# Kernel tuning notes

Measured on AMD Instinct MI355X. Metric: run time of the kernel, lower is better.

## Reference

```python
import jax, jax.numpy as jnp
import numpy as np

DIM = 180
HEADS = 6
WIN = 12
NGS = 2304          # num_gs_seed -> gs len
SQ = 48             # sqrt(num_gs_seed)
B = 64              # window-batch
TABLE = (2 * max(SQ, WIN) - 1) ** 2  # 9025 rows in bias table


def _rel_pos_index():
    # Mirrors the torch __init__ buffer construction (np.unique gives the
    # deterministic sorted-unique indexing the original intends).
    cs = (np.indices((SQ, SQ)) + 0.5) * WIN          # [2, SQ, SQ]
    ct = (np.indices((WIN, WIN)) + 0.5) * SQ
    d = cs.reshape(2, -1)[:, :, None] - ct.reshape(2, -1)[:, None, :]
    _, inv = np.unique(d.flatten(), return_inverse=True)
    idx = inv.reshape(d.shape).astype(np.int64)
    idx[0] *= idx.max()
    return jnp.asarray(idx.sum(0), dtype=jnp.int32)


def setup_inputs() -> dict:
    key = jax.random.key(0)
    ks = jax.random.split(key, 12)
    std = 0.02
    d = DIM
    inp = {
        "gs": jax.random.normal(ks[0], (B, NGS, d), dtype=jnp.float32),
        "feat": jax.random.normal(ks[1], (B, WIN * WIN, d), dtype=jnp.float32),
        "Wq": jax.random.normal(ks[2], (d, d), dtype=jnp.float32) * std,
        "bq": jnp.zeros((d,), dtype=jnp.float32),
        "Wk": jax.random.normal(ks[3], (d, d), dtype=jnp.float32) * std,
        "bk": jnp.zeros((d,), dtype=jnp.float32),
        "Wv": jax.random.normal(ks[4], (d, d), dtype=jnp.float32) * std,
        "bv": jnp.zeros((d,), dtype=jnp.float32),
        "Wp": jax.random.normal(ks[5], (d, d), dtype=jnp.float32) * std,
        "bp": jnp.zeros((d,), dtype=jnp.float32),
        "bias_table": jax.random.normal(ks[6], (TABLE, HEADS), dtype=jnp.float32) * std,
        "rel_pos_index": _rel_pos_index(),
    }
    return inp


def reference(gs, feat, Wq, bq, Wk, bk, Wv, bv, Wp, bp, bias_table, rel_pos_index):
    b, ng, c = gs.shape
    n = feat.shape[1]
    hd = c // HEADS
    scale = hd ** (-0.5)

    q = (gs @ Wq + bq).reshape(b, ng, HEADS, hd).transpose(0, 2, 1, 3) * scale  # [b,H,ng,hd]
    k = (feat @ Wk + bk).reshape(b, n, HEADS, hd).transpose(0, 2, 1, 3)          # [b,H,n,hd]
    v = (feat @ Wv + bv).reshape(b, n, HEADS, hd).transpose(0, 2, 1, 3)

    attn = jnp.einsum('bhqd,bhkd->bhqk', q, k)                                    # [b,H,ng,n]
    bias = bias_table[rel_pos_index]                                              # [ng,n,H]
    attn = attn + jnp.transpose(bias, (2, 0, 1))[None]                            # broadcast over b
    attn = jax.nn.softmax(attn, axis=-1)

    x = jnp.einsum('bhqk,bhkd->bhqd', attn, v)                                    # [b,H,ng,hd]
    x = x.transpose(0, 2, 1, 3).reshape(b, ng, c)
    return x @ Wp + bp
```

## Files before the change

kernel.cpp:

```cpp
#include <hip/hip_runtime.h>

#define DIM   180
#define HEADS 6
#define HD    30
#define NKEY  144
#define NGS   2304
#define BATCH 64
#define TQ    64
#define QT    (NGS / TQ)
#define WPAD  192
#define SXS   200
#define SQS   200
#define SPS   152
#define SVS   152
#define SKS   40
#define KB_STRIDE (NKEY * SKS)
#define VB_STRIDE (32 * SVS)

typedef unsigned short u16;
typedef short v8s __attribute__((ext_vector_type(8)));
typedef float v4f __attribute__((ext_vector_type(4)));

__device__ __forceinline__ float bf2f(u16 u) {
    union { unsigned int i; float f; } w; w.i = ((unsigned int)u) << 16; return w.f;
}
__device__ __forceinline__ u16 f2bf(float f) {
    union { float f; unsigned int i; } w; w.f = f;
    unsigned int r = w.i + 0x7fffu + ((w.i >> 16) & 1u);
    return (u16)(r >> 16);
}

__global__ __launch_bounds__(256) void wt_prep_kernel(
    const float* __restrict__ Wq, const float* __restrict__ Wp,
    u16* __restrict__ WqT, u16* __restrict__ WpT) {
    int idx = blockIdx.x * 256 + threadIdx.x;
    int sel = idx >= WPAD * WPAD;
    int rr  = sel ? idx - WPAD * WPAD : idx;
    int j = rr / WPAD, k = rr - j * WPAD;
    const float* W = sel ? Wp : Wq;
    u16* T = sel ? WpT : WqT;
    float v = (j < DIM && k < DIM) ? W[k * DIM + j] : 0.f;
    T[j * WPAD + k] = f2bf(v);
}

__global__ __launch_bounds__(256) void gather_bias_kernel(
    const float* __restrict__ table, const int* __restrict__ rpi,
    u16* __restrict__ biasg) {
    int idx = blockIdx.x * 256 + threadIdx.x;
    int r = rpi[idx];
    int q = idx / NKEY, n = idx - q * NKEY;
#pragma unroll
    for (int h = 0; h < HEADS; ++h)
        biasg[((size_t)h * NGS + q) * NKEY + n] = f2bf(table[r * HEADS + h]);
}

__global__ __launch_bounds__(256) void kv_proj_kernel(
    const float* __restrict__ feat,
    const float* __restrict__ Wk, const float* __restrict__ bk,
    const float* __restrict__ Wv, const float* __restrict__ bv,
    u16* __restrict__ Kb, u16* __restrict__ VbT) {
    __shared__ float sF[16 * DIM];
    int b  = blockIdx.x / 9;
    int n0 = (blockIdx.x % 9) * 16;
    int tid = threadIdx.x;
    {
        const float4* src = (const float4*)(feat + (size_t)(b * NKEY + n0) * DIM);
        float4* dst = (float4*)sF;
        for (int i = tid; i < 16 * 45; i += 256) dst[i] = src[i];
    }
    __syncthreads();
    int j = tid;
    if (j < DIM) {
        float ak[16], av[16];
#pragma unroll
        for (int r = 0; r < 16; ++r) { ak[r] = 0.f; av[r] = 0.f; }
        const float4* sF4 = (const float4*)sF;
        for (int kc = 0; kc < 45; ++kc) {
            int kk = kc * 4;
            float wk0 = Wk[(kk + 0) * DIM + j], wk1 = Wk[(kk + 1) * DIM + j];
            float wk2 = Wk[(kk + 2) * DIM + j], wk3 = Wk[(kk + 3) * DIM + j];
            float wv0 = Wv[(kk + 0) * DIM + j], wv1 = Wv[(kk + 1) * DIM + j];
            float wv2 = Wv[(kk + 2) * DIM + j], wv3 = Wv[(kk + 3) * DIM + j];
#pragma unroll
            for (int r = 0; r < 16; ++r) {
                float4 g = sF4[r * 45 + kc];
                ak[r] = fmaf(g.x, wk0, ak[r]); ak[r] = fmaf(g.y, wk1, ak[r]);
                ak[r] = fmaf(g.z, wk2, ak[r]); ak[r] = fmaf(g.w, wk3, ak[r]);
                av[r] = fmaf(g.x, wv0, av[r]); av[r] = fmaf(g.y, wv1, av[r]);
                av[r] = fmaf(g.z, wv2, av[r]); av[r] = fmaf(g.w, wv3, av[r]);
            }
        }
        int h = j / 30, d = j - 30 * h;
        u16* kp = Kb  + (size_t)(b * HEADS + h) * KB_STRIDE;
        u16* vp = VbT + (size_t)(b * HEADS + h) * VB_STRIDE;
        float bkj = bk[j], bvj = bv[j];
#pragma unroll
        for (int r = 0; r < 16; ++r) {
            kp[(n0 + r) * SKS + d] = f2bf(ak[r] + bkj);
            vp[d * SVS + n0 + r]   = f2bf(av[r] + bvj);
        }
    }
}

__global__ __launch_bounds__(256, 2) void attn_kernel(
    const float* __restrict__ gs,
    const u16* __restrict__ WqT, const float* __restrict__ bq,
    const u16* __restrict__ WpT, const float* __restrict__ bp,
    const u16* __restrict__ Kb, const u16* __restrict__ VbT,
    const u16* __restrict__ biasg, float* __restrict__ out) {

    __shared__ u16 sX[TQ * SXS];
    __shared__ u16 sQ[TQ * SQS];
    __shared__ u16 sP[TQ * SPS];
    __shared__ u16 sV[32 * SVS];

    const int tid  = threadIdx.x;
    const int w    = tid >> 6;
    const int l15  = tid & 15;
    const int quad = (tid >> 4) & 3;
    const int b    = blockIdx.x / QT;
    const int q0   = (blockIdx.x % QT) * TQ;
    const float SCALE = 0.18257418583505536f;

    {
        const float4* src = (const float4*)(gs + (size_t)(b * NGS + q0) * DIM);
        for (int i = tid; i < TQ * 45; i += 256) {
            int row = i / 45, c = i - row * 45;
            float4 g = src[row * 45 + c];
            unsigned lo = (unsigned)f2bf(g.x) | ((unsigned)f2bf(g.y) << 16);
            unsigned hi = (unsigned)f2bf(g.z) | ((unsigned)f2bf(g.w) << 16);
            *(uint2*)&sX[row * SXS + c * 4] = make_uint2(lo, hi);
        }
        for (int i = tid; i < TQ * 16; i += 256)
            sX[(i >> 4) * SXS + 180 + (i & 15)] = 0;
    }
    __syncthreads();

    {
        v4f acc[12];
#pragma unroll
        for (int i = 0; i < 12; ++i) acc[i] = (v4f){0.f, 0.f, 0.f, 0.f};
        for (int kt = 0; kt < 6; ++kt) {
            v8s A[4];
#pragma unroll
            for (int m = 0; m < 4; ++m)
                A[m] = *(const v8s*)&sX[(16 * m + l15) * SXS + kt * 32 + quad * 8];
#pragma unroll
            for (int jj = 0; jj < 3; ++jj) {
                int j0 = (3 * w + jj) * 16;
                v8s B = *(const v8s*)&WqT[(size_t)(j0 + l15) * WPAD + kt * 32 + quad * 8];
#pragma unroll
                for (int m = 0; m < 4; ++m)
                    acc[jj * 4 + m] = __builtin_amdgcn_mfma_f32_16x16x32_bf16(
                        A[m], B, acc[jj * 4 + m], 0, 0, 0);
            }
        }
#pragma unroll
        for (int jj = 0; jj < 3; ++jj) {
            int j = (3 * w + jj) * 16 + l15;
            if (j < DIM) {
                int h = j / 30;
                int pos = j + 2 * h;
                float bqj = bq[j];
#pragma unroll
                for (int m = 0; m < 4; ++m)
#pragma unroll
                    for (int r = 0; r < 4; ++r)
                        sQ[(16 * m + quad * 4 + r) * SQS + pos] =
                            f2bf((acc[jj * 4 + m][r] + bqj) * SCALE);
            }
        }
    }
    for (int i = tid; i < TQ * HEADS * 2; i += 256) {
        int row = i / 12, c = i - row * 12;
        sQ[row * SQS + (c >> 1) * 32 + 30 + (c & 1)] = 0;
    }
    __syncthreads();

    for (int h = 0; h < HEADS; ++h) {
        {
            const uint4* ks = (const uint4*)(Kb + (size_t)(b * HEADS + h) * KB_STRIDE);
            uint4* kd = (uint4*)sP;
            for (int i = tid; i < (KB_STRIDE * 2 / 16); i += 256) kd[i] = ks[i];
            const uint4* vs = (const uint4*)(VbT + (size_t)(b * HEADS + h) * VB_STRIDE);
            uint4* vd = (uint4*)sV;
            for (int i = tid; i < (VB_STRIDE * 2 / 16); i += 256) vd[i] = vs[i];
        }
        __syncthreads();

        v8s qa = *(const v8s*)&sQ[(16 * w + l15) * SQS + h * 32 + quad * 8];
        v4f la[9];
        const u16* bg = biasg + ((size_t)h * NGS + q0 + 16 * w + quad * 4) * NKEY + l15;
#pragma unroll
        for (int t = 0; t < 9; ++t) {
            v4f c;
#pragma unroll
            for (int r = 0; r < 4; ++r) c[r] = bf2f(bg[r * NKEY + t * 16]);
            v8s kb = *(const v8s*)&sP[(16 * t + l15) * SKS + quad * 8];
            la[t] = __builtin_amdgcn_mfma_f32_16x16x32_bf16(qa, kb, c, 0, 0, 0);
        }

        float mx[4], sm[4];
#pragma unroll
        for (int r = 0; r < 4; ++r) {
            float m = la[0][r];
#pragma unroll
            for (int t = 1; t < 9; ++t) m = fmaxf(m, la[t][r]);
            m = fmaxf(m, __shfl_xor(m, 1));
            m = fmaxf(m, __shfl_xor(m, 2));
            m = fmaxf(m, __shfl_xor(m, 4));
            m = fmaxf(m, __shfl_xor(m, 8));
            mx[r] = m; sm[r] = 0.f;
        }
#pragma unroll
        for (int t = 0; t < 9; ++t)
#pragma unroll
            for (int r = 0; r < 4; ++r) {
                la[t][r] = __expf(la[t][r] - mx[r]);
                sm[r] += la[t][r];
            }
#pragma unroll
        for (int r = 0; r < 4; ++r) {
            sm[r] += __shfl_xor(sm[r], 1);
            sm[r] += __shfl_xor(sm[r], 2);
            sm[r] += __shfl_xor(sm[r], 4);
            sm[r] += __shfl_xor(sm[r], 8);
            sm[r] = 1.f / sm[r];
        }
        __syncthreads();

#pragma unroll
        for (int t = 0; t < 9; ++t)
#pragma unroll
            for (int r = 0; r < 4; ++r)
                sP[(16 * w + quad * 4 + r) * SPS + 16 * t + l15] = f2bf(la[t][r] * sm[r]);
        __syncthreads();

        v4f x0 = (v4f){0.f, 0.f, 0.f, 0.f}, x1 = x0;
        for (int kt = 0; kt < 5; ++kt) {
            v8s pa, vb0, vb1;
            if (kt == 4 && quad >= 2) {
                pa = (v8s){0,0,0,0,0,0,0,0}; vb0 = pa; vb1 = pa;
            } else {
                pa  = *(const v8s*)&sP[(16 * w + l15) * SPS + kt * 32 + quad * 8];
                vb0 = *(const v8s*)&sV[l15 * SVS + kt * 32 + quad * 8];
                vb1 = *(const v8s*)&sV[(16 + l15) * SVS + kt * 32 + quad * 8];
            }
            x0 = __builtin_amdgcn_mfma_f32_16x16x32_bf16(pa, vb0, x0, 0, 0, 0);
            x1 = __builtin_amdgcn_mfma_f32_16x16x32_bf16(pa, vb1, x1, 0, 0, 0);
        }
#pragma unroll
        for (int r = 0; r < 4; ++r) {
            int qrow = (16 * w + quad * 4 + r) * SXS + h * 30;
            sX[qrow + l15] = f2bf(x0[r]);
            if (l15 < 14) sX[qrow + 16 + l15] = f2bf(x1[r]);
        }
        __syncthreads();
    }

    {
        v4f acc[12];
#pragma unroll
        for (int i = 0; i < 12; ++i) acc[i] = (v4f){0.f, 0.f, 0.f, 0.f};
        for (int kt = 0; kt < 6; ++kt) {
            v8s A[4];
#pragma unroll
            for (int m = 0; m < 4; ++m)
                A[m] = *(const v8s*)&sX[(16 * m + l15) * SXS + kt * 32 + quad * 8];
#pragma unroll
            for (int jj = 0; jj < 3; ++jj) {
                int j0 = (3 * w + jj) * 16;
                v8s B = *(const v8s*)&WpT[(size_t)(j0 + l15) * WPAD + kt * 32 + quad * 8];
#pragma unroll
                for (int m = 0; m < 4; ++m)
                    acc[jj * 4 + m] = __builtin_amdgcn_mfma_f32_16x16x32_bf16(
                        A[m], B, acc[jj * 4 + m], 0, 0, 0);
            }
        }
#pragma unroll
        for (int jj = 0; jj < 3; ++jj) {
            int j = (3 * w + jj) * 16 + l15;
            if (j < DIM) {
                float bpj = bp[j];
#pragma unroll
                for (int m = 0; m < 4; ++m)
#pragma unroll
                    for (int r = 0; r < 4; ++r)
                        out[(size_t)(b * NGS + q0 + 16 * m + quad * 4 + r) * DIM + j] =
                            acc[jj * 4 + m][r] + bpj;
            }
        }
    }
}

extern "C" void kernel_launch(void* const* d_in, const int* in_sizes, int n_in,
                              void* d_out, int out_size, void* d_ws, size_t ws_size,
                              hipStream_t stream) {
    const float* gs    = (const float*)d_in[0];
    const float* feat  = (const float*)d_in[1];
    const float* Wq    = (const float*)d_in[2];
    const float* bq    = (const float*)d_in[3];
    const float* Wk    = (const float*)d_in[4];
    const float* bk    = (const float*)d_in[5];
    const float* Wv    = (const float*)d_in[6];
    const float* bv    = (const float*)d_in[7];
    const float* Wp    = (const float*)d_in[8];
    const float* bp    = (const float*)d_in[9];
    const float* table = (const float*)d_in[10];
    const int*   rpi   = (const int*)d_in[11];
    float* out = (float*)d_out;

    u16* WqT   = (u16*)d_ws;
    u16* WpT   = WqT + WPAD * WPAD;
    u16* Kb    = WpT + WPAD * WPAD;
    u16* VbT   = Kb  + (size_t)BATCH * HEADS * KB_STRIDE;
    u16* biasg = VbT + (size_t)BATCH * HEADS * VB_STRIDE;

    size_t zero_bytes = (size_t)BATCH * HEADS * (KB_STRIDE + VB_STRIDE) * sizeof(u16);
    hipMemsetAsync(Kb, 0, zero_bytes, stream);

    wt_prep_kernel<<<dim3(2 * WPAD * WPAD / 256), dim3(256), 0, stream>>>(Wq, Wp, WqT, WpT);
    gather_bias_kernel<<<dim3(NGS * NKEY / 256), dim3(256), 0, stream>>>(table, rpi, biasg);
    kv_proj_kernel<<<dim3(BATCH * 9), dim3(256), 0, stream>>>(feat, Wk, bk, Wv, bv, Kb, VbT);
    attn_kernel<<<dim3(BATCH * QT), dim3(256), 0, stream>>>(
        gs, WqT, bq, WpT, bp, Kb, VbT, biasg, out);
}
```

Before: 447.1 us.

## Read K/V from global directly, transpose attention MFMA, pre-tile bias in fragment order

```diff
diff --git a/kernel.cpp b/kernel.cpp
--- a/kernel.cpp
+++ b/kernel.cpp
@@ -7,15 +7,14 @@
 #define NGS   2304
 #define BATCH 64
 #define TQ    64
-#define QT    (NGS / TQ)
+#define QT    36
 #define WPAD  192
 #define SXS   200
-#define SQS   200
 #define SPS   152
-#define SVS   152
-#define SKS   40
-#define KB_STRIDE (NKEY * SKS)
-#define VB_STRIDE (32 * SVS)
+#define KROW  40
+#define VROW  144
+#define KB_STRIDE (NKEY * KROW)
+#define VB_STRIDE (32 * VROW)
 
 typedef unsigned short u16;
 typedef short v8s __attribute__((ext_vector_type(8)));
@@ -28,6 +27,12 @@
     union { float f; unsigned int i; } w; w.f = f;
     unsigned int r = w.i + 0x7fffu + ((w.i >> 16) & 1u);
     return (u16)(r >> 16);
+}
+__device__ __forceinline__ uint2 pack4(const v4f& x) {
+    uint2 r;
+    r.x = (unsigned)f2bf(x[0]) | ((unsigned)f2bf(x[1]) << 16);
+    r.y = (unsigned)f2bf(x[2]) | ((unsigned)f2bf(x[3]) << 16);
+    return r;
 }
 
 __global__ __launch_bounds__(256) void wt_prep_kernel(
@@ -37,21 +42,35 @@
     int sel = idx >= WPAD * WPAD;
     int rr  = sel ? idx - WPAD * WPAD : idx;
     int j = rr / WPAD, k = rr - j * WPAD;
-    const float* W = sel ? Wp : Wq;
-    u16* T = sel ? WpT : WqT;
-    float v = (j < DIM && k < DIM) ? W[k * DIM + j] : 0.f;
-    T[j * WPAD + k] = f2bf(v);
+    float v;
+    if (!sel) {
+        v = (j < DIM && k < DIM) ? Wq[k * DIM + j] : 0.f;
+        WqT[j * WPAD + k] = f2bf(v);
+    } else {
+        int h = k >> 5, dd = k & 31;
+        v = (j < DIM && dd < HD) ? Wp[(h * HD + dd) * DIM + j] : 0.f;
+        WpT[j * WPAD + k] = f2bf(v);
+    }
 }
 
 __global__ __launch_bounds__(256) void gather_bias_kernel(
     const float* __restrict__ table, const int* __restrict__ rpi,
-    u16* __restrict__ biasg) {
-    int idx = blockIdx.x * 256 + threadIdx.x;
-    int r = rpi[idx];
-    int q = idx / NKEY, n = idx - q * NKEY;
-#pragma unroll
-    for (int h = 0; h < HEADS; ++h)
-        biasg[((size_t)h * NGS + q) * NKEY + n] = f2bf(table[r * HEADS + h]);
+    u16* __restrict__ biasCT) {
+    int i = blockIdx.x * 256 + threadIdx.x;
+    int lane = i & 63;
+    int tile = i >> 6;
+    int t = tile % 9;
+    int rem = tile / 9;
+    int g = rem % 144;
+    int h = rem / 144;
+    int q  = 16 * g + (lane & 15);
+    int n0 = 16 * t + (lane >> 4) * 4;
+    const int4 rr = *(const int4*)&rpi[q * NKEY + n0];
+    unsigned lo = (unsigned)f2bf(table[rr.x * HEADS + h]) |
+                  ((unsigned)f2bf(table[rr.y * HEADS + h]) << 16);
+    unsigned hi = (unsigned)f2bf(table[rr.z * HEADS + h]) |
+                  ((unsigned)f2bf(table[rr.w * HEADS + h]) << 16);
+    ((uint2*)biasCT)[i] = make_uint2(lo, hi);
 }
 
 __global__ __launch_bounds__(256) void kv_proj_kernel(
@@ -90,36 +109,36 @@
                 av[r] = fmaf(g.z, wv2, av[r]); av[r] = fmaf(g.w, wv3, av[r]);
             }
         }
-        int h = j / 30, d = j - 30 * h;
+        int h = j / HD, d = j - HD * h;
         u16* kp = Kb  + (size_t)(b * HEADS + h) * KB_STRIDE;
         u16* vp = VbT + (size_t)(b * HEADS + h) * VB_STRIDE;
         float bkj = bk[j], bvj = bv[j];
 #pragma unroll
         for (int r = 0; r < 16; ++r) {
-            kp[(n0 + r) * SKS + d] = f2bf(ak[r] + bkj);
-            vp[d * SVS + n0 + r]   = f2bf(av[r] + bvj);
-        }
-    }
-}
-
-__global__ __launch_bounds__(256, 2) void attn_kernel(
+            kp[(n0 + r) * KROW + d] = f2bf(ak[r] + bkj);
+            vp[d * VROW + n0 + r]   = f2bf(av[r] + bvj);
+        }
+    }
+}
+
+__global__ __launch_bounds__(256, 3) void attn_kernel(
     const float* __restrict__ gs,
     const u16* __restrict__ WqT, const float* __restrict__ bq,
     const u16* __restrict__ WpT, const float* __restrict__ bp,
     const u16* __restrict__ Kb, const u16* __restrict__ VbT,
-    const u16* __restrict__ biasg, float* __restrict__ out) {
-
-    __shared__ u16 sX[TQ * SXS];
-    __shared__ u16 sQ[TQ * SQS];
+    const u16* __restrict__ biasCT, float* __restrict__ out) {
+
+    __shared__ u16 sXQ[TQ * SXS];
     __shared__ u16 sP[TQ * SPS];
-    __shared__ u16 sV[32 * SVS];
 
     const int tid  = threadIdx.x;
     const int w    = tid >> 6;
+    const int lane = tid & 63;
     const int l15  = tid & 15;
     const int quad = (tid >> 4) & 3;
     const int b    = blockIdx.x / QT;
-    const int q0   = (blockIdx.x % QT) * TQ;
+    const int qt   = blockIdx.x % QT;
+    const int q0   = qt * TQ;
     const float SCALE = 0.18257418583505536f;
 
     {
@@ -129,10 +148,114 @@
             float4 g = src[row * 45 + c];
             unsigned lo = (unsigned)f2bf(g.x) | ((unsigned)f2bf(g.y) << 16);
             unsigned hi = (unsigned)f2bf(g.z) | ((unsigned)f2bf(g.w) << 16);
-            *(uint2*)&sX[row * SXS + c * 4] = make_uint2(lo, hi);
+            *(uint2*)&sXQ[row * SXS + c * 4] = make_uint2(lo, hi);
         }
         for (int i = tid; i < TQ * 16; i += 256)
-            sX[(i >> 4) * SXS + 180 + (i & 15)] = 0;
+            sXQ[(i >> 4) * SXS + 180 + (i & 15)] = 0;
+    }
+    __syncthreads();
+
+    v4f qacc[12];
+#pragma unroll
+    for (int i = 0; i < 12; ++i) qacc[i] = (v4f){0.f, 0.f, 0.f, 0.f};
+    for (int kt = 0; kt < 6; ++kt) {
+        v8s A[4];
+#pragma unroll
+        for (int m = 0; m < 4; ++m)
+            A[m] = *(const v8s*)&sXQ[(16 * m + l15) * SXS + kt * 32 + quad * 8];
+#pragma unroll
+        for (int jj = 0; jj < 3; ++jj) {
+            v8s B = *(const v8s*)&WqT[(size_t)((3 * w + jj) * 16 + l15) * WPAD +
+                                      kt * 32 + quad * 8];
+#pragma unroll
+            for (int m = 0; m < 4; ++m)
+                qacc[jj * 4 + m] = __builtin_amdgcn_mfma_f32_16x16x32_bf16(
+                    A[m], B, qacc[jj * 4 + m], 0, 0, 0);
+        }
+    }
+    __syncthreads();
+#pragma unroll
+    for (int jj = 0; jj < 3; ++jj) {
+        int j = (3 * w + jj) * 16 + l15;
+        if (j < DIM) {
+            int h = j / HD;
+            int pos = j + 2 * h;
+            float bqj = bq[j];
+#pragma unroll
+            for (int m = 0; m < 4; ++m)
+#pragma unroll
+                for (int r = 0; r < 4; ++r)
+                    sXQ[(16 * m + quad * 4 + r) * SXS + pos] =
+                        f2bf((qacc[jj * 4 + m][r] + bqj) * SCALE);
+        }
+    }
+    for (int i = tid; i < TQ * 12; i += 256) {
+        int row = i / 12, c = i - row * 12;
+        sXQ[row * SXS + (c >> 1) * 32 + 30 + (c & 1)] = 0;
+    }
+    __syncthreads();
+
+    for (int h = 0; h < HEADS; ++h) {
+        const u16* kp = Kb  + (size_t)(b * HEADS + h) * KB_STRIDE;
+        const u16* vp = VbT + (size_t)(b * HEADS + h) * VB_STRIDE;
+
+        v8s qa = *(const v8s*)&sXQ[(16 * w + l15) * SXS + h * 32 + quad * 8];
+
+        v4f la[9];
+        const u16* bgt = biasCT +
+            ((size_t)((h * 144 + (qt * 4 + w)) * 9) * 256) + lane * 4;
+#pragma unroll
+        for (int t = 0; t < 9; ++t) {
+            uint2 bb = *(const uint2*)(bgt + t * 256);
+            v4f c;
+            c[0] = bf2f((u16)(bb.x & 0xffff));
+            c[1] = bf2f((u16)(bb.x >> 16));
+            c[2] = bf2f((u16)(bb.y & 0xffff));
+            c[3] = bf2f((u16)(bb.y >> 16));
+            v8s kb = *(const v8s*)&kp[(16 * t + l15) * KROW + quad * 8];
+            la[t] = __builtin_amdgcn_mfma_f32_16x16x32_bf16(kb, qa, c, 0, 0, 0);
+        }
+
+        float m = la[0][0];
+#pragma unroll
+        for (int t = 0; t < 9; ++t)
+#pragma unroll
+            for (int r = 0; r < 4; ++r) m = fmaxf(m, la[t][r]);
+        m = fmaxf(m, __shfl_xor(m, 16));
+        m = fmaxf(m, __shfl_xor(m, 32));
+        float s = 0.f;
+#pragma unroll
+        for (int t = 0; t < 9; ++t)
+#pragma unroll
+            for (int r = 0; r < 4; ++r) {
+                la[t][r] = __expf(la[t][r] - m);
+                s += la[t][r];
+            }
+        s += __shfl_xor(s, 16);
+        s += __shfl_xor(s, 32);
+        float inv = 1.f / s;
+
+#pragma unroll
+        for (int t = 0; t < 9; ++t) {
+            v4f p;
+#pragma unroll
+            for (int r = 0; r < 4; ++r) p[r] = la[t][r] * inv;
+            *(uint2*)&sP[(16 * w + l15) * SPS + 16 * t + quad * 4] = pack4(p);
+        }
+
+        v4f x0 = (v4f){0.f, 0.f, 0.f, 0.f}, x1 = x0;
+        for (int kt = 0; kt < 5; ++kt) {
+            v8s pa = (v8s){0,0,0,0,0,0,0,0}, a0 = pa, a1 = pa;
+            if (!(kt == 4 && quad >= 2)) {
+                pa = *(const v8s*)&sP[(16 * w + l15) * SPS + kt * 32 + quad * 8];
+                a0 = *(const v8s*)&vp[l15 * VROW + kt * 32 + quad * 8];
+                a1 = *(const v8s*)&vp[(16 + l15) * VROW + kt * 32 + quad * 8];
+            }
+            x0 = __builtin_amdgcn_mfma_f32_16x16x32_bf16(a0, pa, x0, 0, 0, 0);
+            x1 = __builtin_amdgcn_mfma_f32_16x16x32_bf16(a1, pa, x1, 0, 0, 0);
+        }
+        *(uint2*)&sXQ[(16 * w + l15) * SXS + h * 32 + quad * 4]      = pack4(x0);
+        *(uint2*)&sXQ[(16 * w + l15) * SXS + h * 32 + 16 + quad * 4] = pack4(x1);
     }
     __syncthreads();
 
@@ -144,133 +267,11 @@
             v8s A[4];
 #pragma unroll
             for (int m = 0; m < 4; ++m)
-                A[m] = *(const v8s*)&sX[(16 * m + l15) * SXS + kt * 32 + quad * 8];
+                A[m] = *(const v8s*)&sXQ[(16 * m + l15) * SXS + kt * 32 + quad * 8];
 #pragma unroll
             for (int jj = 0; jj < 3; ++jj) {
-                int j0 = (3 * w + jj) * 16;
-                v8s B = *(const v8s*)&WqT[(size_t)(j0 + l15) * WPAD + kt * 32 + quad * 8];
-#pragma unroll
-                for (int m = 0; m < 4; ++m)
-                    acc[jj * 4 + m] = __builtin_amdgcn_mfma_f32_16x16x32_bf16(
-                        A[m], B, acc[jj * 4 + m], 0, 0, 0);
-            }
-        }
-#pragma unroll
-        for (int jj = 0; jj < 3; ++jj) {
-            int j = (3 * w + jj) * 16 + l15;
-            if (j < DIM) {
-                int h = j / 30;
-                int pos = j + 2 * h;
-                float bqj = bq[j];
-#pragma unroll
-                for (int m = 0; m < 4; ++m)
-#pragma unroll
-                    for (int r = 0; r < 4; ++r)
-                        sQ[(16 * m + quad * 4 + r) * SQS + pos] =
-                            f2bf((acc[jj * 4 + m][r] + bqj) * SCALE);
-            }
-        }
-    }
-    for (int i = tid; i < TQ * HEADS * 2; i += 256) {
-        int row = i / 12, c = i - row * 12;
-        sQ[row * SQS + (c >> 1) * 32 + 30 + (c & 1)] = 0;
-    }
-    __syncthreads();
-
-    for (int h = 0; h < HEADS; ++h) {
-        {
-            const uint4* ks = (const uint4*)(Kb + (size_t)(b * HEADS + h) * KB_STRIDE);
-            uint4* kd = (uint4*)sP;
-            for (int i = tid; i < (KB_STRIDE * 2 / 16); i += 256) kd[i] = ks[i];
-            const uint4* vs = (const uint4*)(VbT + (size_t)(b * HEADS + h) * VB_STRIDE);
-            uint4* vd = (uint4*)sV;
-            for (int i = tid; i < (VB_STRIDE * 2 / 16); i += 256) vd[i] = vs[i];
-        }
-        __syncthreads();
-
-        v8s qa = *(const v8s*)&sQ[(16 * w + l15) * SQS + h * 32 + quad * 8];
-        v4f la[9];
-        const u16* bg = biasg + ((size_t)h * NGS + q0 + 16 * w + quad * 4) * NKEY + l15;
-#pragma unroll
-        for (int t = 0; t < 9; ++t) {
-            v4f c;
-#pragma unroll
-            for (int r = 0; r < 4; ++r) c[r] = bf2f(bg[r * NKEY + t * 16]);
-            v8s kb = *(const v8s*)&sP[(16 * t + l15) * SKS + quad * 8];
-            la[t] = __builtin_amdgcn_mfma_f32_16x16x32_bf16(qa, kb, c, 0, 0, 0);
-        }
-
-        float mx[4], sm[4];
-#pragma unroll
-        for (int r = 0; r < 4; ++r) {
-            float m = la[0][r];
-#pragma unroll
-            for (int t = 1; t < 9; ++t) m = fmaxf(m, la[t][r]);
-            m = fmaxf(m, __shfl_xor(m, 1));
-            m = fmaxf(m, __shfl_xor(m, 2));
-            m = fmaxf(m, __shfl_xor(m, 4));
-            m = fmaxf(m, __shfl_xor(m, 8));
-            mx[r] = m; sm[r] = 0.f;
-        }
-#pragma unroll
-        for (int t = 0; t < 9; ++t)
-#pragma unroll
-            for (int r = 0; r < 4; ++r) {
-                la[t][r] = __expf(la[t][r] - mx[r]);
-                sm[r] += la[t][r];
-            }
-#pragma unroll
-        for (int r = 0; r < 4; ++r) {
-            sm[r] += __shfl_xor(sm[r], 1);
-            sm[r] += __shfl_xor(sm[r], 2);
-            sm[r] += __shfl_xor(sm[r], 4);
-            sm[r] += __shfl_xor(sm[r], 8);
-            sm[r] = 1.f / sm[r];
-        }
-        __syncthreads();
-
-#pragma unroll
-        for (int t = 0; t < 9; ++t)
-#pragma unroll
-            for (int r = 0; r < 4; ++r)
-                sP[(16 * w + quad * 4 + r) * SPS + 16 * t + l15] = f2bf(la[t][r] * sm[r]);
-        __syncthreads();
-
-        v4f x0 = (v4f){0.f, 0.f, 0.f, 0.f}, x1 = x0;
-        for (int kt = 0; kt < 5; ++kt) {
-            v8s pa, vb0, vb1;
-            if (kt == 4 && quad >= 2) {
-                pa = (v8s){0,0,0,0,0,0,0,0}; vb0 = pa; vb1 = pa;
-            } else {
-                pa  = *(const v8s*)&sP[(16 * w + l15) * SPS + kt * 32 + quad * 8];
-                vb0 = *(const v8s*)&sV[l15 * SVS + kt * 32 + quad * 8];
-                vb1 = *(const v8s*)&sV[(16 + l15) * SVS + kt * 32 + quad * 8];
-            }
-            x0 = __builtin_amdgcn_mfma_f32_16x16x32_bf16(pa, vb0, x0, 0, 0, 0);
-            x1 = __builtin_amdgcn_mfma_f32_16x16x32_bf16(pa, vb1, x1, 0, 0, 0);
-        }
-#pragma unroll
-        for (int r = 0; r < 4; ++r) {
-            int qrow = (16 * w + quad * 4 + r) * SXS + h * 30;
-            sX[qrow + l15] = f2bf(x0[r]);
-            if (l15 < 14) sX[qrow + 16 + l15] = f2bf(x1[r]);
-        }
-        __syncthreads();
-    }
-
-    {
-        v4f acc[12];
-#pragma unroll
-        for (int i = 0; i < 12; ++i) acc[i] = (v4f){0.f, 0.f, 0.f, 0.f};
-        for (int kt = 0; kt < 6; ++kt) {
-            v8s A[4];
-#pragma unroll
-            for (int m = 0; m < 4; ++m)
-                A[m] = *(const v8s*)&sX[(16 * m + l15) * SXS + kt * 32 + quad * 8];
-#pragma unroll
-            for (int jj = 0; jj < 3; ++jj) {
-                int j0 = (3 * w + jj) * 16;
-                v8s B = *(const v8s*)&WpT[(size_t)(j0 + l15) * WPAD + kt * 32 + quad * 8];
+                v8s B = *(const v8s*)&WpT[(size_t)((3 * w + jj) * 16 + l15) * WPAD +
+                                          kt * 32 + quad * 8];
 #pragma unroll
                 for (int m = 0; m < 4; ++m)
                     acc[jj * 4 + m] = __builtin_amdgcn_mfma_f32_16x16x32_bf16(
@@ -310,18 +311,19 @@
     const int*   rpi   = (const int*)d_in[11];
     float* out = (float*)d_out;
 
-    u16* WqT   = (u16*)d_ws;
-    u16* WpT   = WqT + WPAD * WPAD;
-    u16* Kb    = WpT + WPAD * WPAD;
-    u16* VbT   = Kb  + (size_t)BATCH * HEADS * KB_STRIDE;
-    u16* biasg = VbT + (size_t)BATCH * HEADS * VB_STRIDE;
+    u16* WqT    = (u16*)d_ws;
+    u16* WpT    = WqT + WPAD * WPAD;
+    u16* Kb     = WpT + WPAD * WPAD;
+    u16* VbT    = Kb  + (size_t)BATCH * HEADS * KB_STRIDE;
+    u16* biasCT = VbT + (size_t)BATCH * HEADS * VB_STRIDE;
 
     size_t zero_bytes = (size_t)BATCH * HEADS * (KB_STRIDE + VB_STRIDE) * sizeof(u16);
     hipMemsetAsync(Kb, 0, zero_bytes, stream);
 
     wt_prep_kernel<<<dim3(2 * WPAD * WPAD / 256), dim3(256), 0, stream>>>(Wq, Wp, WqT, WpT);
-    gather_bias_kernel<<<dim3(NGS * NKEY / 256), dim3(256), 0, stream>>>(table, rpi, biasg);
+    gather_bias_kernel<<<dim3(HEADS * 144 * 9 * 64 / 256), dim3(256), 0, stream>>>(
+        table, rpi, biasCT);
     kv_proj_kernel<<<dim3(BATCH * 9), dim3(256), 0, stream>>>(feat, Wk, bk, Wv, bv, Kb, VbT);
     attn_kernel<<<dim3(BATCH * QT), dim3(256), 0, stream>>>(
-        gs, WqT, bq, WpT, bp, Kb, VbT, biasg, out);
-}
+        gs, WqT, bq, WpT, bp, Kb, VbT, biasCT, out);
+}
```

New measurement: 381.2 us. 14.7% less time.
